# Kernel optimization log

Measured on AMD Instinct MI355X. Metric: run time of the kernel, lower is better.

Reference implementation:

```python
import jax, jax.numpy as jnp
import numpy as np

N = 50000
E = 500000
NIN, NHID, NOUT = 256, 128, 64


def setup_inputs() -> dict:
    key = jax.random.key(0)
    ks = jax.random.split(key, 6)
    x = jax.random.normal(ks[0], (N, NIN), dtype=jnp.float32)
    edge_index = jax.random.randint(ks[1], (2, E), 0, N, dtype=jnp.int64)
    # GCNConv weights (glorot-ish scale) and biases
    W1 = jax.random.normal(ks[2], (NIN, NHID), dtype=jnp.float32) / np.sqrt(NIN)
    b1 = jnp.zeros((NHID,), dtype=jnp.float32)
    W2 = jax.random.normal(ks[3], (NHID, NHID), dtype=jnp.float32) / np.sqrt(NHID)
    b2 = jnp.zeros((NHID,), dtype=jnp.float32)
    # decoder Linear
    Wd = jax.random.normal(ks[4], (NHID, NOUT), dtype=jnp.float32) / np.sqrt(NHID)
    bd = jnp.zeros((NOUT,), dtype=jnp.float32)
    return {"x": x, "edge_index": edge_index, "W1": W1, "b1": b1,
            "W2": W2, "b2": b2, "Wd": Wd, "bd": bd}


def _gcn_norm(edge_index, n):
    # add self-loops, then symmetric normalization deg^-1/2 * deg^-1/2
    loops = jnp.arange(n, dtype=edge_index.dtype)
    src = jnp.concatenate([edge_index[0], loops])
    dst = jnp.concatenate([edge_index[1], loops])
    deg = jax.ops.segment_sum(jnp.ones_like(dst, dtype=jnp.float32), dst,
                              num_segments=n)
    dis = jnp.where(deg > 0, jax.lax.rsqrt(deg), 0.0)
    norm = dis[src] * dis[dst]  # [E + N]
    return src, dst, norm


def _gcn_conv(h, W, b, src, dst, norm, n):
    h = h @ W                              # [N, out]
    msg = h[src] * norm[:, None]           # gather + scale  [E+N, out]
    agg = jax.ops.segment_sum(msg, dst, num_segments=n)  # scatter-add
    return agg + b


def reference(x, edge_index, W1, b1, W2, b2, Wd, bd):
    n = x.shape[0]
    src, dst, norm = _gcn_norm(edge_index, n)
    h = jax.nn.relu(_gcn_conv(x, W1, b1, src, dst, norm, n))
    h = jax.nn.relu(_gcn_conv(h, W2, b2, src, dst, norm, n))
    # dropout is a no-op in eval mode
    out = h @ Wd + bd
    return out, h
```

## Files before the change

kernel.cpp:

```cpp
#include <hip/hip_runtime.h>

#define NIN 256
#define NHID 128
#define NOUT 64
#define CAP 64
#define CSTRIDE 16

typedef __attribute__((ext_vector_type(8))) short bf16x8;
typedef __attribute__((ext_vector_type(4))) float f32x4;

__device__ __forceinline__ unsigned int bf16_rne(float v) {
    unsigned int b = __float_as_uint(v);
    return (b + 0x7fffu + ((b >> 16) & 1u)) >> 16;
}
__device__ __forceinline__ float bf16_to_f(unsigned int bits16) {
    return __uint_as_float(bits16 << 16);
}

__device__ __forceinline__ void pack_dev(const float* __restrict__ W,
                                         uint4* __restrict__ hi, uint4* __restrict__ lo,
                                         int K, int N, int idx) {
    int lane = idx & 63;
    int f = idx >> 6;
    int nct = N / 16;
    int ct = f % nct;
    int kt = f / nct;
    int col = ct * 16 + (lane & 15);
    int k0 = kt * 32 + (lane >> 4) * 8;
    unsigned int hs[8], ls[8];
#pragma unroll
    for (int e = 0; e < 8; ++e) {
        float v = W[(size_t)(k0 + e) * N + col];
        unsigned int h = bf16_rne(v);
        float hf = __uint_as_float(h << 16);
        ls[e] = bf16_rne(v - hf);
        hs[e] = h;
    }
    uint4 hv, lv;
    hv.x = hs[0] | (hs[1] << 16); hv.y = hs[2] | (hs[3] << 16);
    hv.z = hs[4] | (hs[5] << 16); hv.w = hs[6] | (hs[7] << 16);
    lv.x = ls[0] | (ls[1] << 16); lv.y = ls[2] | (ls[3] << 16);
    lv.z = ls[4] | (ls[5] << 16); lv.w = ls[6] | (ls[7] << 16);
    hi[idx] = hv;
    lo[idx] = lv;
}

__global__ __launch_bounds__(256) void setup_kernel(int* __restrict__ cursor,
                                                    const float* __restrict__ W1,
                                                    const float* __restrict__ W2,
                                                    const float* __restrict__ Wd,
                                                    uint4* __restrict__ w1hi, uint4* __restrict__ w1lo,
                                                    uint4* __restrict__ w2hi, uint4* __restrict__ w2lo,
                                                    uint4* __restrict__ wdhi, uint4* __restrict__ wdlo,
                                                    int n, int GZ) {
    int bid = blockIdx.x;
    int t = threadIdx.x;
    if (bid < GZ) {
        int i = bid * 256 + t;
        if (i < n * CSTRIDE) cursor[i] = 0;
    } else {
        int pidx = (bid - GZ) * 256 + t;
        if (pidx < 4096)       pack_dev(W1, w1hi, w1lo, NIN,  NHID, pidx);
        else if (pidx < 6144)  pack_dev(W2, w2hi, w2lo, NHID, NHID, pidx - 4096);
        else                   pack_dev(Wd, wdhi, wdlo, NHID, NOUT, pidx - 6144);
    }
}

__global__ __launch_bounds__(256) void mega_kernel(const float* __restrict__ x,
                                                   const int* __restrict__ src,
                                                   const int* __restrict__ dst,
                                                   int* __restrict__ cursor,
                                                   int* __restrict__ bucket,
                                                   const uint4* __restrict__ Bhi,
                                                   const uint4* __restrict__ Blo,
                                                   unsigned int* __restrict__ bufA,
                                                   int n, int E, int GG) {
    constexpr int NKT = NIN / 32;
    constexpr int NCT = NHID / 16;
    __shared__ uint4 lds_b[2][NCT][64];

    int bid = blockIdx.x;
    int t = threadIdx.x;

    if (bid >= GG) {
        int base = (bid - GG) * 1024 + t;
#pragma unroll
        for (int u = 0; u < 4; ++u) {
            int e = base + u * 256;
            if (e < E) {
                int d = dst[e];
                int pos = atomicAdd(&cursor[(size_t)d * CSTRIDE], 1);
                if (pos < CAP) bucket[(size_t)d * CAP + pos] = src[e];
            }
        }
        return;
    }

    int lane = t & 63;
    int w = t >> 6;
    int row0 = bid * 64 + w * 16;
    bool rowok = row0 < n;
    int arow = row0 + (lane & 15);
    int kbase = (lane >> 4) * 8;

    f32x4 acc[NCT];
#pragma unroll
    for (int c = 0; c < NCT; ++c)
#pragma unroll
        for (int r = 0; r < 4; ++r) acc[c][r] = 0.f;

    for (int kt = 0; kt < NKT; ++kt) {
        __syncthreads();
        {
            const uint4* sh = Bhi + (size_t)kt * NCT * 64;
            const uint4* sl = Blo + (size_t)kt * NCT * 64;
            uint4* dh = &lds_b[0][0][0];
            uint4* dl = &lds_b[1][0][0];
            for (int i = t; i < NCT * 64; i += 256) {
                dh[i] = sh[i];
                dl[i] = sl[i];
            }
        }
        __syncthreads();

        bf16x8 ahi, alo;
        {
            float va[8];
            if (rowok) {
                const float* xp = x + (size_t)arow * NIN + kt * 32 + kbase;
                float4 v0 = *(const float4*)xp;
                float4 v1 = *(const float4*)(xp + 4);
                va[0] = v0.x; va[1] = v0.y; va[2] = v0.z; va[3] = v0.w;
                va[4] = v1.x; va[5] = v1.y; va[6] = v1.z; va[7] = v1.w;
            } else {
#pragma unroll
                for (int e = 0; e < 8; ++e) va[e] = 0.f;
            }
#pragma unroll
            for (int e = 0; e < 8; ++e) {
                unsigned int h = bf16_rne(va[e]);
                float hf = __uint_as_float(h << 16);
                unsigned int l = bf16_rne(va[e] - hf);
                ahi[e] = (short)h;
                alo[e] = (short)l;
            }
        }

#pragma unroll
        for (int c = 0; c < NCT; ++c) {
            bf16x8 bhi = *(const bf16x8*)&lds_b[0][c][lane];
            bf16x8 blo = *(const bf16x8*)&lds_b[1][c][lane];
            acc[c] = __builtin_amdgcn_mfma_f32_16x16x32_bf16(ahi, bhi, acc[c], 0, 0, 0);
            acc[c] = __builtin_amdgcn_mfma_f32_16x16x32_bf16(ahi, blo, acc[c], 0, 0, 0);
            acc[c] = __builtin_amdgcn_mfma_f32_16x16x32_bf16(alo, bhi, acc[c], 0, 0, 0);
        }
    }

    if (rowok) {
        int rbase = row0 + (lane >> 4) * 4;
        int cbase = lane & 15;
        unsigned short* Y = (unsigned short*)bufA;
#pragma unroll
        for (int c = 0; c < NCT; ++c) {
            int col = c * 16 + cbase;
#pragma unroll
            for (int r = 0; r < 4; ++r)
                Y[(size_t)(rbase + r) * NHID + col] = (unsigned short)bf16_rne(acc[c][r]);
        }
    }
}

template<int K, int NCOL, bool BIAS, bool XBF, bool OBF>
__global__ __launch_bounds__(256) void gemm_mfma_kernel(const void* __restrict__ Xv,
                                                        const uint4* __restrict__ Bhi,
                                                        const uint4* __restrict__ Blo,
                                                        const float* __restrict__ bias,
                                                        void* __restrict__ Yv, int nrows) {
    constexpr int NKT = K / 32;
    constexpr int NCT = NCOL / 16;
    __shared__ uint4 lds_b[2][NCT][64];

    int t = threadIdx.x;
    int lane = t & 63;
    int w = t >> 6;
    int row0 = blockIdx.x * 64 + w * 16;
    bool rowok = row0 < nrows;
    int arow = row0 + (lane & 15);
    int kbase = (lane >> 4) * 8;

    f32x4 acc[NCT];
#pragma unroll
    for (int c = 0; c < NCT; ++c)
#pragma unroll
        for (int r = 0; r < 4; ++r) acc[c][r] = 0.f;

    for (int kt = 0; kt < NKT; ++kt) {
        __syncthreads();
        {
            const uint4* sh = Bhi + (size_t)kt * NCT * 64;
            const uint4* sl = Blo + (size_t)kt * NCT * 64;
            uint4* dh = &lds_b[0][0][0];
            uint4* dl = &lds_b[1][0][0];
            for (int i = t; i < NCT * 64; i += 256) {
                dh[i] = sh[i];
                dl[i] = sl[i];
            }
        }
        __syncthreads();

        bf16x8 ahi, alo;
        if constexpr (XBF) {
            const unsigned short* X = (const unsigned short*)Xv;
            if (rowok)
                ahi = *(const bf16x8*)(X + (size_t)arow * K + kt * 32 + kbase);
            else
#pragma unroll
                for (int e = 0; e < 8; ++e) ahi[e] = 0;
        } else {
            const float* X = (const float*)Xv;
            float va[8];
            if (rowok) {
                const float* xp = X + (size_t)arow * K + kt * 32 + kbase;
                float4 v0 = *(const float4*)xp;
                float4 v1 = *(const float4*)(xp + 4);
                va[0] = v0.x; va[1] = v0.y; va[2] = v0.z; va[3] = v0.w;
                va[4] = v1.x; va[5] = v1.y; va[6] = v1.z; va[7] = v1.w;
            } else {
#pragma unroll
                for (int e = 0; e < 8; ++e) va[e] = 0.f;
            }
#pragma unroll
            for (int e = 0; e < 8; ++e) {
                unsigned int h = bf16_rne(va[e]);
                float hf = __uint_as_float(h << 16);
                unsigned int l = bf16_rne(va[e] - hf);
                ahi[e] = (short)h;
                alo[e] = (short)l;
            }
        }

#pragma unroll
        for (int c = 0; c < NCT; ++c) {
            bf16x8 bhi = *(const bf16x8*)&lds_b[0][c][lane];
            bf16x8 blo = *(const bf16x8*)&lds_b[1][c][lane];
            acc[c] = __builtin_amdgcn_mfma_f32_16x16x32_bf16(ahi, bhi, acc[c], 0, 0, 0);
            acc[c] = __builtin_amdgcn_mfma_f32_16x16x32_bf16(ahi, blo, acc[c], 0, 0, 0);
            if constexpr (!XBF)
                acc[c] = __builtin_amdgcn_mfma_f32_16x16x32_bf16(alo, bhi, acc[c], 0, 0, 0);
        }
    }

    if (rowok) {
        int rbase = row0 + (lane >> 4) * 4;
        int cbase = lane & 15;
#pragma unroll
        for (int c = 0; c < NCT; ++c) {
            int col = c * 16 + cbase;
            float bv = BIAS ? bias[col] : 0.f;
#pragma unroll
            for (int r = 0; r < 4; ++r) {
                float v = acc[c][r] + bv;
                if constexpr (OBF)
                    ((unsigned short*)Yv)[(size_t)(rbase + r) * NCOL + col] =
                        (unsigned short)bf16_rne(v);
                else
                    ((float*)Yv)[(size_t)(rbase + r) * NCOL + col] = v;
            }
        }
    }
}

__global__ __launch_bounds__(256) void agg_kernel(const unsigned int* __restrict__ Hb,
                                                  const int* __restrict__ cursor,
                                                  const int* __restrict__ bucket,
                                                  const float* __restrict__ bias,
                                                  unsigned int* __restrict__ Yb,
                                                  float* __restrict__ Yf, int n) {
    int node = (blockIdx.x * 256 + threadIdx.x) >> 6;
    int lane = threadIdx.x & 63;
    if (node >= n) return;

    int deg = cursor[(size_t)node * CSTRIDE];
    float di = rsqrtf((float)(deg + 1));
    unsigned int su = Hb[(size_t)node * 64 + lane];
    int c = min(deg, CAP);

    int s = 0;
    float wl = 0.f;
    if (lane < c) {
        s = bucket[(size_t)node * CAP + lane];
        wl = rsqrtf((float)(cursor[(size_t)s * CSTRIDE] + 1));
    }

    float ax[8], ay[8];
#pragma unroll
    for (int u = 0; u < 8; ++u) { ax[u] = 0.f; ay[u] = 0.f; }
    ax[0] = bf16_to_f(su & 0xffffu) * di;
    ay[0] = bf16_to_f(su >> 16) * di;

    for (int jj = 0; jj < c; jj += 8) {
        int   sv[8];
        float wv[8];
#pragma unroll
        for (int u = 0; u < 8; ++u) {
            sv[u] = __shfl(s, jj + u, 64);
            wv[u] = __shfl(wl, jj + u, 64);
        }
        unsigned int vv[8];
#pragma unroll
        for (int u = 0; u < 8; ++u)
            vv[u] = Hb[(size_t)sv[u] * 64 + lane];
#pragma unroll
        for (int u = 0; u < 8; ++u) {
            ax[u] += bf16_to_f(vv[u] & 0xffffu) * wv[u];
            ay[u] += bf16_to_f(vv[u] >> 16) * wv[u];
        }
    }

    float2 b = ((const float2*)bias)[lane];
    float rx = (((ax[0] + ax[1]) + (ax[2] + ax[3])) + ((ax[4] + ax[5]) + (ax[6] + ax[7]))) * di + b.x;
    float ry = (((ay[0] + ay[1]) + (ay[2] + ay[3])) + ((ay[4] + ay[5]) + (ay[6] + ay[7]))) * di + b.y;
    rx = fmaxf(rx, 0.f);
    ry = fmaxf(ry, 0.f);
    Yb[(size_t)node * 64 + lane] = bf16_rne(rx) | (bf16_rne(ry) << 16);
    if (Yf) {
        float2 o; o.x = rx; o.y = ry;
        ((float2*)(Yf + (size_t)node * NHID))[lane] = o;
    }
}


extern "C" void kernel_launch(void* const* d_in, const int* in_sizes, int n_in,
                              void* d_out, int out_size, void* d_ws, size_t ws_size,
                              hipStream_t stream) {
    const float* x  = (const float*)d_in[0];
    const int*   ei = (const int*)d_in[1];
    const float* W1 = (const float*)d_in[2];
    const float* b1 = (const float*)d_in[3];
    const float* W2 = (const float*)d_in[4];
    const float* b2 = (const float*)d_in[5];
    const float* Wd = (const float*)d_in[6];
    const float* bd = (const float*)d_in[7];

    int n = in_sizes[0] / NIN;
    int E = in_sizes[1] / 2;
    const int* src = ei;
    const int* dst = ei + E;

    char* ws = (char*)d_ws;
    size_t off = 0;
    auto alloc = [&](size_t bytes) -> void* {
        void* p = ws + off;
        off += (bytes + 255) & ~(size_t)255;
        return p;
    };
    int*   cursor = (int*)alloc((size_t)n * CSTRIDE * 4);
    int*   bucket = (int*)alloc((size_t)n * CAP * 4);
    unsigned int* bufA = (unsigned int*)alloc((size_t)n * 64 * 4);
    unsigned int* h1b  = (unsigned int*)alloc((size_t)n * 64 * 4);
    unsigned int* bufB = (unsigned int*)alloc((size_t)n * 64 * 4);
    unsigned int* h2b  = (unsigned int*)alloc((size_t)n * 64 * 4);
    uint4* w1hi = (uint4*)alloc((size_t)(NIN / 32) * (NHID / 16) * 64 * 16);
    uint4* w1lo = (uint4*)alloc((size_t)(NIN / 32) * (NHID / 16) * 64 * 16);
    uint4* w2hi = (uint4*)alloc((size_t)(NHID / 32) * (NHID / 16) * 64 * 16);
    uint4* w2lo = (uint4*)alloc((size_t)(NHID / 32) * (NHID / 16) * 64 * 16);
    uint4* wdhi = (uint4*)alloc((size_t)(NHID / 32) * (NOUT / 16) * 64 * 16);
    uint4* wdlo = (uint4*)alloc((size_t)(NHID / 32) * (NOUT / 16) * 64 * 16);

    float* out  = (float*)d_out;
    float* hout = out + (size_t)n * NOUT;

    int GZ = (n * CSTRIDE + 255) / 256;
    int GG = (n + 63) / 64;
    int GF = (E + 1023) / 1024;
    int gGemm = GG;
    int gAgg = (n + 3) / 4;

    setup_kernel<<<GZ + 28, 256, 0, stream>>>(cursor, W1, W2, Wd,
                                              w1hi, w1lo, w2hi, w2lo, wdhi, wdlo, n, GZ);

    mega_kernel<<<GG + GF, 256, 0, stream>>>(x, src, dst, cursor, bucket,
                                             w1hi, w1lo, bufA, n, E, GG);

    agg_kernel<<<gAgg, 256, 0, stream>>>(bufA, cursor, bucket, b1, h1b, nullptr, n);

    gemm_mfma_kernel<NHID, NHID, false, true, true><<<gGemm, 256, 0, stream>>>(
        h1b, w2hi, w2lo, nullptr, bufB, n);
    agg_kernel<<<gAgg, 256, 0, stream>>>(bufB, cursor, bucket, b2, h2b, hout, n);

    gemm_mfma_kernel<NHID, NOUT, true, true, false><<<gGemm, 256, 0, stream>>>(
        h2b, wdhi, wdlo, bd, out, n);
}
```

Before: 124.2 us.

## Split per-node edge buckets into 16 block-indexed sub-buckets and precompute degree norms

The edge binning now spreads each destination's atomic counter across 16 slots chosen by block index, so atomics on the same node from different blocks hit different addresses, and it stores sources in 16 sub-buckets of capacity 16. A new small kernel sums the 16 counters per node into a precomputed deg^-1/2 array. The aggregation kernel reads 16 counters per node to compact the sub-buckets into lane order and looks up the neighbor norm from that array instead of a strided cursor read. This adds a kernel launch, 16 counter loads per node in each aggregation pass, and a bucket array four times larger, and truncation now happens per sub-bucket rather than per node.

```diff
diff --git a/kernel.cpp b/kernel.cpp
--- a/kernel.cpp
+++ b/kernel.cpp
@@ -3,8 +3,8 @@
 #define NIN 256
 #define NHID 128
 #define NOUT 64
-#define CAP 64
-#define CSTRIDE 16
+#define NCLS 16
+#define CAP16 16
 
 typedef __attribute__((ext_vector_type(8))) short bf16x8;
 typedef __attribute__((ext_vector_type(4))) float f32x4;
@@ -45,7 +45,7 @@
     lo[idx] = lv;
 }
 
-__global__ __launch_bounds__(256) void setup_kernel(int* __restrict__ cursor,
+__global__ __launch_bounds__(256) void setup_kernel(int* __restrict__ cursor16,
                                                     const float* __restrict__ W1,
                                                     const float* __restrict__ W2,
                                                     const float* __restrict__ Wd,
@@ -57,7 +57,7 @@
     int t = threadIdx.x;
     if (bid < GZ) {
         int i = bid * 256 + t;
-        if (i < n * CSTRIDE) cursor[i] = 0;
+        if (i < n * NCLS) cursor16[i] = 0;
     } else {
         int pidx = (bid - GZ) * 256 + t;
         if (pidx < 4096)       pack_dev(W1, w1hi, w1lo, NIN,  NHID, pidx);
@@ -69,8 +69,8 @@
 __global__ __launch_bounds__(256) void mega_kernel(const float* __restrict__ x,
                                                    const int* __restrict__ src,
                                                    const int* __restrict__ dst,
-                                                   int* __restrict__ cursor,
-                                                   int* __restrict__ bucket,
+                                                   int* __restrict__ cursor16,
+                                                   int* __restrict__ bucket16,
                                                    const uint4* __restrict__ Bhi,
                                                    const uint4* __restrict__ Blo,
                                                    unsigned int* __restrict__ bufA,
@@ -83,14 +83,16 @@
     int t = threadIdx.x;
 
     if (bid >= GG) {
+        int cls = bid & (NCLS - 1);
         int base = (bid - GG) * 1024 + t;
 #pragma unroll
         for (int u = 0; u < 4; ++u) {
             int e = base + u * 256;
             if (e < E) {
                 int d = dst[e];
-                int pos = atomicAdd(&cursor[(size_t)d * CSTRIDE], 1);
-                if (pos < CAP) bucket[(size_t)d * CAP + pos] = src[e];
+                size_t slot = (size_t)d * NCLS + cls;
+                int pos = atomicAdd(&cursor16[slot], 1);
+                if (pos < CAP16) bucket16[slot * CAP16 + pos] = src[e];
             }
         }
         return;
@@ -168,6 +170,20 @@
                 Y[(size_t)(rbase + r) * NHID + col] = (unsigned short)bf16_rne(acc[c][r]);
         }
     }
+}
+
+__global__ __launch_bounds__(256) void deg_dis_kernel(const int* __restrict__ cursor16,
+                                                      float* __restrict__ dis, int n) {
+    int i = blockIdx.x * 256 + threadIdx.x;
+    if (i >= n) return;
+    const int4* p = (const int4*)(cursor16 + (size_t)i * NCLS);
+    int s = 0;
+#pragma unroll
+    for (int q = 0; q < NCLS / 4; ++q) {
+        int4 v = p[q];
+        s += v.x + v.y + v.z + v.w;
+    }
+    dis[i] = rsqrtf((float)(s + 1));
 }
 
 template<int K, int NCOL, bool BIAS, bool XBF, bool OBF>
@@ -270,9 +286,11 @@
     }
 }
 
+
 __global__ __launch_bounds__(256) void agg_kernel(const unsigned int* __restrict__ Hb,
-                                                  const int* __restrict__ cursor,
-                                                  const int* __restrict__ bucket,
+                                                  const int* __restrict__ cursor16,
+                                                  const int* __restrict__ bucket16,
+                                                  const float* __restrict__ dis,
                                                   const float* __restrict__ bias,
                                                   unsigned int* __restrict__ Yb,
                                                   float* __restrict__ Yf, int n) {
@@ -280,16 +298,24 @@
     int lane = threadIdx.x & 63;
     if (node >= n) return;
 
-    int deg = cursor[(size_t)node * CSTRIDE];
-    float di = rsqrtf((float)(deg + 1));
+    float di = dis[node];
     unsigned int su = Hb[(size_t)node * 64 + lane];
-    int c = min(deg, CAP);
+
+    int ksel = -1, jsel = 0, P = 0;
+#pragma unroll
+    for (int k = 0; k < NCLS; ++k) {
+        int ck = cursor16[(size_t)node * NCLS + k];
+        ck = min(ck, CAP16);
+        if (lane >= P && lane < P + ck) { ksel = k; jsel = lane - P; }
+        P += ck;
+    }
+    int cnt = P;
 
     int s = 0;
     float wl = 0.f;
-    if (lane < c) {
-        s = bucket[(size_t)node * CAP + lane];
-        wl = rsqrtf((float)(cursor[(size_t)s * CSTRIDE] + 1));
+    if (ksel >= 0) {
+        s = bucket16[((size_t)node * NCLS + ksel) * CAP16 + jsel];
+        wl = dis[s];
     }
 
     float ax[8], ay[8];
@@ -298,7 +324,7 @@
     ax[0] = bf16_to_f(su & 0xffffu) * di;
     ay[0] = bf16_to_f(su >> 16) * di;
 
-    for (int jj = 0; jj < c; jj += 8) {
+    for (int jj = 0; jj < cnt; jj += 8) {
         int   sv[8];
         float wv[8];
 #pragma unroll
@@ -354,8 +380,9 @@
         off += (bytes + 255) & ~(size_t)255;
         return p;
     };
-    int*   cursor = (int*)alloc((size_t)n * CSTRIDE * 4);
-    int*   bucket = (int*)alloc((size_t)n * CAP * 4);
+    int*   cursor16 = (int*)alloc((size_t)n * NCLS * 4);
+    int*   bucket16 = (int*)alloc((size_t)n * NCLS * CAP16 * 4);
+    float* dis      = (float*)alloc((size_t)n * 4);
     unsigned int* bufA = (unsigned int*)alloc((size_t)n * 64 * 4);
     unsigned int* h1b  = (unsigned int*)alloc((size_t)n * 64 * 4);
     unsigned int* bufB = (unsigned int*)alloc((size_t)n * 64 * 4);
@@ -370,23 +397,26 @@
     float* out  = (float*)d_out;
     float* hout = out + (size_t)n * NOUT;
 
-    int GZ = (n * CSTRIDE + 255) / 256;
+    int GZ = (n * NCLS + 255) / 256;
     int GG = (n + 63) / 64;
     int GF = (E + 1023) / 1024;
     int gGemm = GG;
     int gAgg = (n + 3) / 4;
-
-    setup_kernel<<<GZ + 28, 256, 0, stream>>>(cursor, W1, W2, Wd,
+    int gN = (n + 255) / 256;
+
+    setup_kernel<<<GZ + 28, 256, 0, stream>>>(cursor16, W1, W2, Wd,
                                               w1hi, w1lo, w2hi, w2lo, wdhi, wdlo, n, GZ);
 
-    mega_kernel<<<GG + GF, 256, 0, stream>>>(x, src, dst, cursor, bucket,
+    mega_kernel<<<GG + GF, 256, 0, stream>>>(x, src, dst, cursor16, bucket16,
                                              w1hi, w1lo, bufA, n, E, GG);
 
-    agg_kernel<<<gAgg, 256, 0, stream>>>(bufA, cursor, bucket, b1, h1b, nullptr, n);
+    deg_dis_kernel<<<gN, 256, 0, stream>>>(cursor16, dis, n);
+
+    agg_kernel<<<gAgg, 256, 0, stream>>>(bufA, cursor16, bucket16, dis, b1, h1b, nullptr, n);
 
     gemm_mfma_kernel<NHID, NHID, false, true, true><<<gGemm, 256, 0, stream>>>(
         h1b, w2hi, w2lo, nullptr, bufB, n);
-    agg_kernel<<<gAgg, 256, 0, stream>>>(bufB, cursor, bucket, b2, h2b, hout, n);
+    agg_kernel<<<gAgg, 256, 0, stream>>>(bufB, cursor16, bucket16, dis, b2, h2b, hout, n);
 
     gemm_mfma_kernel<NHID, NOUT, true, true, false><<<gGemm, 256, 0, stream>>>(
         h2b, wdhi, wdlo, bd, out, n);
```

After: 126.4 us. No clear change (+1.8%).
